# Optimization experiments

Measured on AMD Instinct MI355X. Metric: run time of the kernel, lower is better.

The kernel has to match this reference:

```python
import jax, jax.numpy as jnp
import numpy as np

NUM_BINS = 32
FAIRNESS_PENALTY = 0.1
SENSITIVE = (0, 5)


def setup_inputs() -> dict:
    key = jax.random.key(0)
    k1, k2, k3, k4 = jax.random.split(key, 4)
    B, F, P = 65536, 256, 32
    x = jax.random.uniform(k1, (B, F), dtype=jnp.float32)  # features in [0,1)
    W = jax.random.normal(k2, (F, NUM_BINS), dtype=jnp.float32) * 0.1  # main-effect weights
    IW = jax.random.normal(k3, (P, NUM_BINS, NUM_BINS), dtype=jnp.float32) * 0.1  # pairwise weights
    intercept = jax.random.normal(k4, (1,), dtype=jnp.float32)
    # build(): feature_bins[i] = linspace(0, 1, num_bins+1) for every feature
    bins = jnp.tile(jnp.linspace(0.0, 1.0, NUM_BINS + 1, dtype=jnp.float32)[None, :], (F, 1))
    pair_i = jnp.arange(P, dtype=jnp.int32) * 2  # interaction_terms = [(0,1),(2,3),...]
    pair_j = pair_i + 1
    return dict(x=x, W=W, IW=IW, intercept=intercept, bins=bins, pair_i=pair_i, pair_j=pair_j)


def _bin_indices(x, bins):
    # x: [B,F], bins: [F,NB+1] -> int32 [B,F]; matches tf sum(x>=bins)-1 with clip
    idx = jnp.sum((x[:, :, None] >= bins[None, :, :]).astype(jnp.int32), axis=-1) - 1
    return jnp.clip(idx, 0, NUM_BINS - 1)


def reference(x, W, IW, intercept, bins, pair_i, pair_j):
    B, F = x.shape
    P = IW.shape[0]
    idx = _bin_indices(x, bins)  # [B,F]
    main = W[jnp.arange(F)[None, :], idx]  # per-feature gathered contributions [B,F]
    inter = IW[jnp.arange(P)[None, :], idx[:, pair_i], idx[:, pair_j]]  # [B,P]
    preds = intercept[0] + main.sum(axis=1) + inter.sum(axis=1)  # [B]
    fairness_loss = FAIRNESS_PENALTY * sum(jnp.var(main[:, s]) for s in SENSITIVE)
    return preds[:, None], fairness_loss
```

## Files before the change

### kernel.cpp

```cpp
#include <hip/hip_runtime.h>


#define F        256
#define NBINS    32
#define PPAIRS   32
#define WPB      8
#define BLOCK    (WPB * 64)
#define GRID     1024
#define ROWS     8
#define WPAD     (NBINS + 1)

template <int ctrl, int row_mask, int bank_mask>
__device__ __forceinline__ float dpp_add(float x) {
    int y = __builtin_amdgcn_update_dpp(0, __float_as_int(x), ctrl, row_mask, bank_mask, false);
    return x + __int_as_float(y);
}

__device__ __forceinline__ float wave_sum_lane63(float x) {
    x = dpp_add<0x111, 0xf, 0xf>(x);
    x = dpp_add<0x112, 0xf, 0xf>(x);
    x = dpp_add<0x114, 0xf, 0xe>(x);
    x = dpp_add<0x118, 0xf, 0xc>(x);
    x = dpp_add<0x142, 0xa, 0xf>(x);
    x = dpp_add<0x143, 0x8, 0xf>(x);
    return x;
}

__global__ __launch_bounds__(BLOCK, 4) void febm_main(
    const float* __restrict__ x, const float* __restrict__ W,
    const float* __restrict__ IW, const float* __restrict__ intercept,
    float* __restrict__ out, float4* __restrict__ partials)
{
    __shared__ float Wl[F * WPAD];
    __shared__ float4 mm[WPB];

    {
        const float4* W4 = (const float4*)W;
        for (int i = threadIdx.x; i < F * NBINS / 4; i += BLOCK) {
            const float4 v = W4[i];
            const int f = i >> 3, k4 = (i & 7) * 4;
            float* dst = &Wl[f * WPAD + k4];
            dst[0] = v.x; dst[1] = v.y; dst[2] = v.z; dst[3] = v.w;
        }
    }
    __syncthreads();

    const int lane = threadIdx.x & 63;
    const int wave = threadIdx.x >> 6;
    const int gw = blockIdx.x * WPB + wave;
    const int base = gw * ROWS;

    const float c0 = intercept[0];

    const float4* xr = (const float4*)x;
    float4 xv[ROWS];
    #pragma unroll
    for (int r = 0; r < ROWS; ++r)
        xv[r] = xr[(size_t)(base + r) * (F / 4) + lane];

    float msum[ROWS], iv[ROWS];
    float sA = 0.f, ssA = 0.f;
    #pragma unroll
    for (int r = 0; r < ROWS; ++r) {
        const float xe[4] = {xv[r].x, xv[r].y, xv[r].z, xv[r].w};
        float acc = 0.f, wf = 0.f;
        unsigned packed = 0;
        #pragma unroll
        for (int i = 0; i < 4; ++i) {
            int k = (int)(xe[i] * 32.0f);
            k = k < 0 ? 0 : (k > NBINS - 1 ? NBINS - 1 : k);
            const float w = Wl[(lane * 4 + i) * WPAD + k];
            acc += w;
            packed |= (unsigned)k << (i * 8);
            if (i == 0) wf = w;
            if (i == 1 && lane == 1) wf = w;
        }
        msum[r] = acc;
        if (lane < 2) { sA += wf; ssA += wf * wf; }

        const unsigned u = (unsigned)__shfl((int)packed, lane >> 1);
        float t = 0.f;
        if (lane < PPAIRS) {
            const int sh = (lane & 1) * 16;
            const int ki = (u >> sh) & 0xff;
            const int kj = (u >> (sh + 8)) & 0xff;
            t = IW[lane * (NBINS * NBINS) + ki * NBINS + kj];
        }
        iv[r] = t;
    }

    float res[ROWS];
    #pragma unroll
    for (int r = 0; r < ROWS; ++r)
        res[r] = c0 + wave_sum_lane63(msum[r] + iv[r]);
    if (lane == 63) {
        ((float4*)(out + base))[0] = make_float4(res[0], res[1], res[2], res[3]);
        ((float4*)(out + base))[1] = make_float4(res[4], res[5], res[6], res[7]);
    }

    if (lane == 0) { mm[wave].x = sA; mm[wave].y = ssA; }
    if (lane == 1) { mm[wave].z = sA; mm[wave].w = ssA; }
    __syncthreads();
    if (threadIdx.x == 0) {
        float4 a = mm[0];
        #pragma unroll
        for (int w = 1; w < WPB; ++w) {
            a.x += mm[w].x; a.y += mm[w].y; a.z += mm[w].z; a.w += mm[w].w;
        }
        partials[blockIdx.x] = a;
    }
}

__global__ __launch_bounds__(256) void febm_reduce(
    const float4* __restrict__ partials, int nPart, float* __restrict__ fair_out, int B)
{
    __shared__ float4 sw[4];
    const int lane = threadIdx.x & 63;
    const int wave = threadIdx.x >> 6;

    float4 a = make_float4(0.f, 0.f, 0.f, 0.f);
    for (int i = threadIdx.x; i < nPart; i += 256) {
        const float4 p = partials[i];
        a.x += p.x; a.y += p.y; a.z += p.z; a.w += p.w;
    }
    #pragma unroll
    for (int off = 32; off > 0; off >>= 1) {
        a.x += __shfl_xor(a.x, off);
        a.y += __shfl_xor(a.y, off);
        a.z += __shfl_xor(a.z, off);
        a.w += __shfl_xor(a.w, off);
    }
    if (lane == 0) sw[wave] = a;
    __syncthreads();
    if (threadIdx.x == 0) {
        float4 t = sw[0];
        #pragma unroll
        for (int w = 1; w < 4; ++w) {
            t.x += sw[w].x; t.y += sw[w].y; t.z += sw[w].z; t.w += sw[w].w;
        }
        const double invB = 1.0 / (double)B;
        const double mean0 = t.x * invB, mean5 = t.z * invB;
        const double var0 = t.y * invB - mean0 * mean0;
        const double var5 = t.w * invB - mean5 * mean5;
        fair_out[0] = (float)(0.1 * (var0 + var5));
    }
}

extern "C" void kernel_launch(void* const* d_in, const int* in_sizes, int n_in,
                              void* d_out, int out_size, void* d_ws, size_t ws_size,
                              hipStream_t stream)
{
    const float* x         = (const float*)d_in[0];
    const float* W         = (const float*)d_in[1];
    const float* IW        = (const float*)d_in[2];
    const float* intercept = (const float*)d_in[3];

    float* out = (float*)d_out;
    const int B = in_sizes[0] / F;
    float4* partials = (float4*)d_ws;

    febm_main<<<GRID, BLOCK, 0, stream>>>(x, W, IW, intercept, out, partials);
    febm_reduce<<<1, 256, 0, stream>>>(partials, GRID, out + B, B);
}
```

Baseline: 111.9 us.

## Process 16 rows per wave in two batches, issuing IW gathers before LDS lookups

Each wave now handles 16 rows instead of 8, and the grid is halved. All 16 row loads are issued up front. Bin indices and the global IW gathers for both batches are computed first, and the LDS weight lookups and wave reductions come afterwards. The aim is to overlap the latency of the global gathers with the shared-memory work and to amortize the per-block W staging over more rows. The cost is higher register pressure and fewer total waves available to hide latency.

Result: no change. 113.6 us (+1.5%).

```diff
diff --git a/kernel.cpp b/kernel.cpp
--- a/kernel.cpp
+++ b/kernel.cpp
@@ -6,8 +6,8 @@
 #define PPAIRS   32
 #define WPB      8
 #define BLOCK    (WPB * 64)
-#define GRID     1024
-#define ROWS     8
+#define GRID     512
+#define BATCH    8
 #define WPAD     (NBINS + 1)
 
 template <int ctrl, int row_mask, int bank_mask>
@@ -48,54 +48,102 @@
     const int lane = threadIdx.x & 63;
     const int wave = threadIdx.x >> 6;
     const int gw = blockIdx.x * WPB + wave;
-    const int base = gw * ROWS;
-
+    const int base = gw * (2 * BATCH);
     const float c0 = intercept[0];
 
     const float4* xr = (const float4*)x;
-    float4 xv[ROWS];
-    #pragma unroll
-    for (int r = 0; r < ROWS; ++r)
-        xv[r] = xr[(size_t)(base + r) * (F / 4) + lane];
-
-    float msum[ROWS], iv[ROWS];
-    float sA = 0.f, ssA = 0.f;
-    #pragma unroll
-    for (int r = 0; r < ROWS; ++r) {
-        const float xe[4] = {xv[r].x, xv[r].y, xv[r].z, xv[r].w};
-        float acc = 0.f, wf = 0.f;
+
+    float4 xv1[BATCH], xv2[BATCH];
+    #pragma unroll
+    for (int r = 0; r < BATCH; ++r)
+        xv1[r] = xr[(size_t)(base + r) * (F / 4) + lane];
+    #pragma unroll
+    for (int r = 0; r < BATCH; ++r)
+        xv2[r] = xr[(size_t)(base + BATCH + r) * (F / 4) + lane];
+
+    unsigned pk1[BATCH], pk2[BATCH];
+    float iv1[BATCH], iv2[BATCH];
+
+    #pragma unroll
+    for (int r = 0; r < BATCH; ++r) {
+        const float xe[4] = {xv1[r].x, xv1[r].y, xv1[r].z, xv1[r].w};
         unsigned packed = 0;
         #pragma unroll
         for (int i = 0; i < 4; ++i) {
             int k = (int)(xe[i] * 32.0f);
             k = k < 0 ? 0 : (k > NBINS - 1 ? NBINS - 1 : k);
-            const float w = Wl[(lane * 4 + i) * WPAD + k];
-            acc += w;
             packed |= (unsigned)k << (i * 8);
-            if (i == 0) wf = w;
-            if (i == 1 && lane == 1) wf = w;
-        }
-        msum[r] = acc;
-        if (lane < 2) { sA += wf; ssA += wf * wf; }
-
+        }
+        pk1[r] = packed;
         const unsigned u = (unsigned)__shfl((int)packed, lane >> 1);
         float t = 0.f;
         if (lane < PPAIRS) {
             const int sh = (lane & 1) * 16;
-            const int ki = (u >> sh) & 0xff;
-            const int kj = (u >> (sh + 8)) & 0xff;
-            t = IW[lane * (NBINS * NBINS) + ki * NBINS + kj];
-        }
-        iv[r] = t;
-    }
-
-    float res[ROWS];
-    #pragma unroll
-    for (int r = 0; r < ROWS; ++r)
-        res[r] = c0 + wave_sum_lane63(msum[r] + iv[r]);
+            t = IW[lane * (NBINS * NBINS) + ((u >> sh) & 0xff) * NBINS
+                   + ((u >> (sh + 8)) & 0xff)];
+        }
+        iv1[r] = t;
+    }
+    #pragma unroll
+    for (int r = 0; r < BATCH; ++r) {
+        const float xe[4] = {xv2[r].x, xv2[r].y, xv2[r].z, xv2[r].w};
+        unsigned packed = 0;
+        #pragma unroll
+        for (int i = 0; i < 4; ++i) {
+            int k = (int)(xe[i] * 32.0f);
+            k = k < 0 ? 0 : (k > NBINS - 1 ? NBINS - 1 : k);
+            packed |= (unsigned)k << (i * 8);
+        }
+        pk2[r] = packed;
+        const unsigned u = (unsigned)__shfl((int)packed, lane >> 1);
+        float t = 0.f;
+        if (lane < PPAIRS) {
+            const int sh = (lane & 1) * 16;
+            t = IW[lane * (NBINS * NBINS) + ((u >> sh) & 0xff) * NBINS
+                   + ((u >> (sh + 8)) & 0xff)];
+        }
+        iv2[r] = t;
+    }
+
+    float sA = 0.f, ssA = 0.f;
+    float res[BATCH];
+
+    #pragma unroll
+    for (int r = 0; r < BATCH; ++r) {
+        float acc = 0.f, wf = 0.f;
+        #pragma unroll
+        for (int i = 0; i < 4; ++i) {
+            const int k = (pk1[r] >> (i * 8)) & 0xff;
+            const float w = Wl[(lane * 4 + i) * WPAD + k];
+            acc += w;
+            if (i == 0) wf = w;
+            if (i == 1 && lane == 1) wf = w;
+        }
+        if (lane < 2) { sA += wf; ssA += wf * wf; }
+        res[r] = c0 + wave_sum_lane63(acc + iv1[r]);
+    }
     if (lane == 63) {
         ((float4*)(out + base))[0] = make_float4(res[0], res[1], res[2], res[3]);
         ((float4*)(out + base))[1] = make_float4(res[4], res[5], res[6], res[7]);
+    }
+
+    #pragma unroll
+    for (int r = 0; r < BATCH; ++r) {
+        float acc = 0.f, wf = 0.f;
+        #pragma unroll
+        for (int i = 0; i < 4; ++i) {
+            const int k = (pk2[r] >> (i * 8)) & 0xff;
+            const float w = Wl[(lane * 4 + i) * WPAD + k];
+            acc += w;
+            if (i == 0) wf = w;
+            if (i == 1 && lane == 1) wf = w;
+        }
+        if (lane < 2) { sA += wf; ssA += wf * wf; }
+        res[r] = c0 + wave_sum_lane63(acc + iv2[r]);
+    }
+    if (lane == 63) {
+        ((float4*)(out + base))[2] = make_float4(res[0], res[1], res[2], res[3]);
+        ((float4*)(out + base))[3] = make_float4(res[4], res[5], res[6], res[7]);
     }
 
     if (lane == 0) { mm[wave].x = sA; mm[wave].y = ssA; }
```
